# Optimization experiments

Measured on AMD Instinct MI355X. Metric: run time of the kernel, lower is better.

Reference implementation:

```python
import jax, jax.numpy as jnp
import numpy as np

NUM_HEADS = 8
NUM_LEVELS = 4
NUM_POINTS = 16
NUM_BEV = 2
EMBED = 256
BS = 64
NQ = NUM_LEVELS * NUM_POINTS  # 64


def _bilinear_sample(img, grid):
    """F.grid_sample(mode='bilinear', padding_mode='zeros', align_corners=False).
    img: (N, C, H, W); grid: (N, Hg, Wg, 2) in [-1, 1] (x, y). Returns (N, C, Hg, Wg)."""
    N, C, H, W = img.shape
    gx = (grid[..., 0] + 1.0) * (W * 0.5) - 0.5  # (N, Hg, Wg)
    gy = (grid[..., 1] + 1.0) * (H * 0.5) - 0.5
    x0 = jnp.floor(gx)
    y0 = jnp.floor(gy)
    flat = img.reshape(N, C, H * W)

    def gather(xi, yi):
        valid = (xi >= 0) & (xi <= W - 1) & (yi >= 0) & (yi <= H - 1)
        xc = jnp.clip(xi, 0, W - 1).astype(jnp.int32)
        yc = jnp.clip(yi, 0, H - 1).astype(jnp.int32)
        idx = (yc * W + xc).reshape(N, 1, -1)
        g = jnp.take_along_axis(flat, idx, axis=2).reshape(N, C, xi.shape[1], xi.shape[2])
        return g * valid[:, None, :, :].astype(img.dtype)

    wx1 = (gx - x0)[:, None]  # (N,1,Hg,Wg)
    wy1 = (gy - y0)[:, None]
    v00 = gather(x0, y0)
    v01 = gather(x0 + 1.0, y0)
    v10 = gather(x0, y0 + 1.0)
    v11 = gather(x0 + 1.0, y0 + 1.0)
    top = v00 * (1.0 - wx1) + v01 * wx1
    bot = v10 * (1.0 - wx1) + v11 * wx1
    return top * (1.0 - wy1) + bot * wy1


def _forward(query, key_hist, value_hist, reference_points, W_off, b_off, spatial_shapes):
    bs, nq, d = query.shape
    Hn, L, P, BEV = NUM_HEADS, NUM_LEVELS, NUM_POINTS, NUM_BEV
    dh = d // Hn
    Pb = P * BEV
    ss = np.asarray(spatial_shapes)  # (L, 2) static (h, w)

    queries = jnp.concatenate([query, query], axis=1)           # (bs, 2*nq, d)
    keies = jnp.concatenate([query, key_hist], axis=1)
    values = jnp.concatenate([query, value_hist], axis=1)
    qb = queries.shape[1]

    # sampling offsets projection (the only used learned linear in the original forward)
    off = (queries @ W_off + b_off).reshape(bs, qb, Hn, Pb, L, 2)

    # NOTE: original re-assigns q/k/v from the RAW concatenated tensors (to_Q/to_K/to_V discarded)
    qh = queries.reshape(bs, qb, Hn, dh)
    kh = keies.reshape(bs, qb, Hn, dh)
    vh = values.reshape(bs, qb, Hn, dh)

    attn = jax.nn.softmax(jnp.einsum('bqhd,bkhd->bqhk', qh, kh), axis=-1)
    attn = attn.reshape(bs, qb, Hn, L, Pb)

    rp = jnp.concatenate([reference_points, reference_points], axis=1)  # (bs, qb, L, 2)
    norm = jnp.stack([jnp.asarray(ss[:, 1], jnp.float32),
                      jnp.asarray(ss[:, 0], jnp.float32)], axis=-1)      # (L, 2) = (w, h)
    loc = rp[:, :, None, None, :, :] + off / norm                        # (bs,qb,H,Pb,L,2)
    # FAITHFUL: original uses .view here (pure reshape, not a transpose)
    loc = loc.reshape(bs, qb, Hn, L, Pb, 2)
    grids = 2.0 * loc - 1.0

    sampled = []
    start = 0
    for l in range(L):
        h_, w_ = int(ss[l, 0]), int(ss[l, 1])
        vl = vh[:, start:start + h_ * w_]                                # (bs, hw, H, dh)
        start += h_ * w_
        img = vl.transpose(0, 2, 3, 1).reshape(bs * Hn, dh, h_, w_)      # (bs*H, dh, h, w)
        grid_l = grids[:, :, :, l].transpose(0, 2, 1, 3, 4).reshape(bs * Hn, qb, Pb, 2)
        sampled.append(_bilinear_sample(img, grid_l))                    # (bs*H, dh, qb, Pb)

    samp = jnp.stack(sampled, axis=-2).reshape(bs * Hn, dh, qb, L * Pb)
    aw = attn.transpose(0, 2, 1, 3, 4).reshape(bs * Hn, 1, qb, L * Pb)
    out = (samp * aw).sum(-1)                                            # (bs*H, dh, qb)
    # FAITHFUL: original reshapes q_bev dim as (nq, BEV) and means over BEV
    out = out.reshape(bs, Hn * dh, nq, BEV).mean(-1).transpose(0, 2, 1)  # (bs, nq, d)
    return out + query  # dropout is identity at eval


def setup_inputs() -> dict:
    key = jax.random.key(0)
    ks = jax.random.split(key, 6)
    query = jax.random.normal(ks[0], (BS, NQ, EMBED), jnp.float32)
    key_hist = jax.random.normal(ks[1], (BS, NQ, EMBED), jnp.float32)
    value_hist = jax.random.normal(ks[2], (BS, NQ, EMBED), jnp.float32)
    reference_points = jax.random.uniform(ks[3], (BS, NQ, NUM_LEVELS, 2), jnp.float32)
    spatial_shapes = jnp.array([[4, 8]] * NUM_LEVELS, dtype=jnp.int32)  # sum(h*w)=128=L*P*BEV
    off_dim = NUM_HEADS * NUM_BEV * NUM_POINTS * NUM_LEVELS * 2
    W_off = jax.random.normal(ks[4], (EMBED, off_dim), jnp.float32) * 0.02
    b_off = jnp.zeros((off_dim,), jnp.float32)
    return {"query": query, "key_hist": key_hist, "value_hist": value_hist,
            "reference_points": reference_points, "spatial_shapes": spatial_shapes,
            "W_off": W_off, "b_off": b_off}


def reference(query, key_hist, value_hist, reference_points, spatial_shapes, W_off, b_off):
    return _forward(query, key_hist, value_hist, reference_points, W_off, b_off, spatial_shapes)
```

## Files before the change

### kernel.cpp

```cpp
#include <hip/hip_runtime.h>


typedef short  s16x8 __attribute__((ext_vector_type(8)));
typedef short  s16x4 __attribute__((ext_vector_type(4)));
typedef float  f32x4 __attribute__((ext_vector_type(4)));

__device__ __forceinline__ unsigned short f2bf(float f) {
    union { float f; unsigned u; } v; v.f = f;
    unsigned r = v.u + 0x7FFFu + ((v.u >> 16) & 1u);
    return (unsigned short)(r >> 16);
}

__global__ __launch_bounds__(256) void prep(
    const float* __restrict__ query, const float* __restrict__ key_hist,
    const float* __restrict__ value_hist,
    short* __restrict__ Ab, short* __restrict__ Khb, short* __restrict__ VTg)
{
    const int job = blockIdx.x, t = threadIdx.x;
    if (job < 2048) {
        const bool isK = job >= 1024;
        const float* src = isK ? key_hist : query;
        short* dst = isK ? Khb : Ab;
        const int i4 = ((job & 1023) * 256 + t) * 4;
        const float4 v = *(const float4*)(src + i4);
        s16x4 o;
        o.x = (short)f2bf(v.x); o.y = (short)f2bf(v.y);
        o.z = (short)f2bf(v.z); o.w = (short)f2bf(v.w);
        *(s16x4*)(dst + i4) = o;
    } else {
        const int bh = job - 2048;
        const int b = bh >> 3, h = bh & 7;
        #pragma unroll
        for (int pass = 0; pass < 4; ++pass) {
            const int idx = t + 256 * pass;
            const int p = idx >> 3;
            const int dg = idx & 7;
            const float* src = (p < 64) ? query : value_hist;
            const float4 v = *(const float4*)(src +
                (size_t)(b * 64 + (p & 63)) * 256 + h * 32 + dg * 4);
            short* o = VTg + ((size_t)bh * 32 + dg * 4) * 128 + p;
            o[0 * 128] = (short)f2bf(v.x);
            o[1 * 128] = (short)f2bf(v.y);
            o[2 * 128] = (short)f2bf(v.z);
            o[3 * 128] = (short)f2bf(v.w);
        }
    }
}

__global__ __launch_bounds__(256) void offs_gemm_mfma(
    const short* __restrict__ Ab, const float* __restrict__ W,
    const float* __restrict__ bias, short* __restrict__ OFFb)
{
    __shared__ __align__(16) short smem[128 * 136];
    short (*Asl)[40] = (short (*)[40])smem;
    short (*Bsl)[40] = (short (*)[40])(smem + 128 * 40);
    short (*Cst)[136] = (short (*)[136])smem;

    const int n0 = blockIdx.x * 128, m0 = blockIdx.y * 128;
    const int t = threadIdx.x, lane = t & 63, wave = t >> 6;
    const int wm0 = (wave >> 1) * 64, wn0 = (wave & 1) * 64;
    const int r = lane & 15, q = lane >> 4;

    f32x4 acc[4][4] = {};

    for (int kc = 0; kc < 256; kc += 32) {
        #pragma unroll
        for (int ss = 0; ss < 2; ++ss) {
            const int seg = t + ss * 256;
            const int row = seg >> 2, off8 = (seg & 3) * 8;
            *(s16x8*)&Asl[row][off8] =
                *(const s16x8*)(Ab + (size_t)(m0 + row) * 256 + kc + off8);
        }
        #pragma unroll
        for (int i = 0; i < 4; ++i) {
            const int slot = t + 256 * i;
            const int kk = slot >> 5, n4 = (slot & 31) * 4;
            const float4 w4 = *(const float4*)(W + (size_t)(kc + kk) * 2048 + n0 + n4);
            Bsl[n4 + 0][kk] = (short)f2bf(w4.x);
            Bsl[n4 + 1][kk] = (short)f2bf(w4.y);
            Bsl[n4 + 2][kk] = (short)f2bf(w4.z);
            Bsl[n4 + 3][kk] = (short)f2bf(w4.w);
        }
        __syncthreads();
        s16x8 af[4], bf[4];
        #pragma unroll
        for (int i = 0; i < 4; ++i) {
            af[i] = *(const s16x8*)&Asl[wm0 + i * 16 + r][q * 8];
            bf[i] = *(const s16x8*)&Bsl[wn0 + i * 16 + r][q * 8];
        }
        #pragma unroll
        for (int i = 0; i < 4; ++i)
            #pragma unroll
            for (int j = 0; j < 4; ++j)
                acc[i][j] = __builtin_amdgcn_mfma_f32_16x16x32_bf16(
                    af[i], bf[j], acc[i][j], 0, 0, 0);
        __syncthreads();
    }

    #pragma unroll
    for (int j = 0; j < 4; ++j) {
        const float bb = bias[n0 + wn0 + j * 16 + r];
        #pragma unroll
        for (int i = 0; i < 4; ++i)
            #pragma unroll
            for (int rg = 0; rg < 4; ++rg)
                Cst[wm0 + i * 16 + q * 4 + rg][wn0 + j * 16 + r] =
                    (short)f2bf(acc[i][j][rg] + bb);
    }
    __syncthreads();
    {
        const int row = t >> 1, half = t & 1;
        short* gdst = OFFb + (size_t)(m0 + row) * 2048 + n0 + half * 64;
        const short* lsrc = &Cst[row][half * 64];
        #pragma unroll
        for (int u = 0; u < 8; ++u)
            *(s16x8*)(gdst + u * 8) = *(const s16x8*)(lsrc + u * 8);
    }
}

__global__ __launch_bounds__(256) void fused_tsa2(
    const float* __restrict__ query, const float* __restrict__ refp,
    const short* __restrict__ Ab, const short* __restrict__ Khb,
    const short* __restrict__ VTg, const unsigned* __restrict__ OFFu,
    float* __restrict__ out)
{
    const int h = blockIdx.x, b = blockIdx.y;
    const int t = threadIdx.x, lane = t & 63, wave = t >> 6;
    const int quad = lane >> 4, col = lane & 15;
    const int wq = wave * 16;

    __shared__ __align__(16) float Am[64][132];
    short* Amb = (short*)&Am[0][0];

    unsigned off_u[8][4];
    {
        const unsigned* ob = OFFu + ((size_t)b * 64 + wq + quad * 4) * 1024 + h * 128 + col;
        #pragma unroll
        for (int r = 0; r < 4; ++r)
            #pragma unroll
            for (int t8 = 0; t8 < 8; ++t8)
                off_u[t8][r] = ob[r * 1024 + t8 * 16];
    }
    float rpx[4], rpy[4];
    #pragma unroll
    for (int r = 0; r < 4; ++r) {
        const float2 rp = *(const float2*)(refp +
            ((size_t)b * 64 + wq + quad * 4 + r) * 8 + (lane & 3) * 2);
        rpx[r] = rp.x; rpy[r] = rp.y;
    }

    {
        const int zq = t >> 2, zc = (t & 3) * 32;
        const float4 z = {0.f, 0.f, 0.f, 0.f};
        #pragma unroll
        for (int u = 0; u < 8; ++u) *(float4*)&Am[zq][zc + 4 * u] = z;
    }

    const s16x8 aq = *(const s16x8*)(Ab +
        ((size_t)b * 64 + wq + col) * 256 + h * 32 + quad * 8);
    f32x4 acc[8];
    #pragma unroll
    for (int t8 = 0; t8 < 8; ++t8) {
        const int n = t8 * 16 + col;
        const short* src = (t8 < 4)
            ? (Ab  + ((size_t)b * 64 + n) * 256)
            : (Khb + ((size_t)b * 64 + n - 64) * 256);
        const s16x8 bk = *(const s16x8*)(src + h * 32 + quad * 8);
        const f32x4 z = {0.f, 0.f, 0.f, 0.f};
        acc[t8] = __builtin_amdgcn_mfma_f32_16x16x32_bf16(aq, bk, z, 0, 0, 0);
    }

    float att[8][4];
    #pragma unroll
    for (int r = 0; r < 4; ++r) {
        float m = acc[0][r];
        #pragma unroll
        for (int t8 = 1; t8 < 8; ++t8) m = fmaxf(m, acc[t8][r]);
        #pragma unroll
        for (int s = 1; s < 16; s <<= 1) m = fmaxf(m, __shfl_xor(m, s, 64));
        float ssum = 0.f;
        #pragma unroll
        for (int t8 = 0; t8 < 8; ++t8) {
            const float e = __expf(acc[t8][r] - m);
            att[t8][r] = e; ssum += e;
        }
        #pragma unroll
        for (int s = 1; s < 16; s <<= 1) ssum += __shfl_xor(ssum, s, 64);
        const float inv = 1.0f / ssum;
        #pragma unroll
        for (int t8 = 0; t8 < 8; ++t8) att[t8][r] *= inv;
    }
    __syncthreads();

    #pragma unroll
    for (int t8 = 0; t8 < 8; ++t8) {
        const int f = col + 16 * t8;
        const int base = (f >> 5) * 32;
        #pragma unroll
        for (int r = 0; r < 4; ++r) {
            float* rowW = &Am[wq + quad * 4 + r][0];
            const float a = att[t8][r];
            const unsigned u = off_u[t8][r];
            const float ox = __uint_as_float(u << 16);
            const float oy = __uint_as_float(u & 0xFFFF0000u);
            const float gx = 8.f * (rpx[r] + ox * 0.125f) - 0.5f;
            const float gy = 4.f * (rpy[r] + oy * 0.25f) - 0.5f;
            const float x0f = floorf(gx), y0f = floorf(gy);
            const float wx = gx - x0f, wy = gy - y0f;
            const int x0 = (int)x0f, y0 = (int)y0f;
            const bool xv0 = (x0 >= 0) && (x0 < 8);
            const bool xv1 = (x0 >= -1) && (x0 < 7);
            const bool yv0 = (y0 >= 0) && (y0 < 4);
            const bool yv1 = (y0 >= -1) && (y0 < 3);
            if (xv0 && yv0) atomicAdd(&rowW[base + y0 * 8 + x0],           a * (1.f - wx) * (1.f - wy));
            if (xv1 && yv0) atomicAdd(&rowW[base + y0 * 8 + x0 + 1],       a * wx * (1.f - wy));
            if (xv0 && yv1) atomicAdd(&rowW[base + (y0 + 1) * 8 + x0],     a * (1.f - wx) * wy);
            if (xv1 && yv1) atomicAdd(&rowW[base + (y0 + 1) * 8 + x0 + 1], a * wx * wy);
        }
    }
    __syncthreads();

    {
        const int cq = t >> 2, cc = (t & 3) * 32;
        float vreg[32];
        #pragma unroll
        for (int u = 0; u < 8; ++u) {
            const float4 v = *(const float4*)&Am[cq][cc + 4 * u];
            vreg[4 * u + 0] = v.x; vreg[4 * u + 1] = v.y;
            vreg[4 * u + 2] = v.z; vreg[4 * u + 3] = v.w;
        }
        __syncthreads();
        #pragma unroll
        for (int u = 0; u < 4; ++u) {
            s16x8 o;
            #pragma unroll
            for (int j = 0; j < 8; ++j) o[j] = (short)f2bf(vreg[u * 8 + j]);
            *(s16x8*)&Amb[cq * 136 + cc + u * 8] = o;
        }
    }
    __syncthreads();

    f32x4 oacc[2] = {};
    #pragma unroll
    for (int ks = 0; ks < 4; ++ks) {
        const s16x8 af = *(const s16x8*)&Amb[(wq + col) * 136 + ks * 32 + quad * 8];
        #pragma unroll
        for (int n2 = 0; n2 < 2; ++n2) {
            const s16x8 bv = *(const s16x8*)(VTg +
                ((size_t)(b * 8 + h) * 32 + n2 * 16 + col) * 128 + ks * 32 + quad * 8);
            oacc[n2] = __builtin_amdgcn_mfma_f32_16x16x32_bf16(af, bv, oacc[n2], 0, 0, 0);
        }
    }

    #pragma unroll
    for (int n2 = 0; n2 < 2; ++n2) {
        const int d = h * 32 + n2 * 16 + col;
        #pragma unroll
        for (int pr = 0; pr < 2; ++pr) {
            const float avg = 0.5f * (oacc[n2][2 * pr] + oacc[n2][2 * pr + 1]);
            const int pj = wave * 8 + quad * 2 + pr;
            const size_t re = ((size_t)b * 64 + pj) * 256 + d;
            const size_t ro = ((size_t)b * 64 + pj + 32) * 256 + d;
            out[re] = query[re] + avg;
            out[ro] = query[ro] + avg;
        }
    }
}

extern "C" void kernel_launch(void* const* d_in, const int* in_sizes, int n_in,
                              void* d_out, int out_size, void* d_ws, size_t ws_size,
                              hipStream_t stream) {
    (void)in_sizes; (void)n_in; (void)out_size; (void)ws_size;
    const float* query      = (const float*)d_in[0];
    const float* key_hist   = (const float*)d_in[1];
    const float* value_hist = (const float*)d_in[2];
    const float* refp       = (const float*)d_in[3];
    const float* W_off      = (const float*)d_in[5];
    const float* b_off      = (const float*)d_in[6];

    char* ws = (char*)d_ws;
    short* Ab   = (short*)(ws);
    short* Khb  = (short*)(ws + (2u << 20));
    short* VTg  = (short*)(ws + (4u << 20));
    short* OFFb = (short*)(ws + (8u << 20));
    float* out  = (float*)d_out;

    prep<<<2560, 256, 0, stream>>>(query, key_hist, value_hist, Ab, Khb, VTg);
    offs_gemm_mfma<<<dim3(16, 32), 256, 0, stream>>>(Ab, W_off, b_off, OFFb);
    fused_tsa2<<<dim3(8, 64), 256, 0, stream>>>(query, refp, Ab, Khb, VTg,
                                                (const unsigned*)OFFb, out);
}
```

Measured before the change: 187.3 us.

## Fuse offset GEMM, bf16 conversion and sampling into one per-head kernel

Replaces the three-kernel pipeline (prep conversion, full offsets GEMM writing bf16 offsets to global, fused attention) with a weight transpose/convert kernel plus a single mega kernel per (head, batch). Each block converts its query/key/value slices to bf16 in LDS, computes its head's slice of the offset projection with MFMA, and consumes the offsets directly from registers for the bilinear-weight scatter. This removes the global round trip of the large offsets tensor and the intermediate bf16 buffers. The cost is heavy LDS use that limits occupancy to one block per CU, and every block of a batch redundantly converts the full query row.

```diff
diff --git a/kernel.cpp b/kernel.cpp
--- a/kernel.cpp
+++ b/kernel.cpp
@@ -11,117 +11,28 @@
     return (unsigned short)(r >> 16);
 }
 
-__global__ __launch_bounds__(256) void prep(
+__global__ __launch_bounds__(256) void transp_bf16(const float* __restrict__ W,
+                                                   short* __restrict__ Wt) {
+    __shared__ float s[32][33];
+    const int n0 = blockIdx.x * 32, k0 = blockIdx.y * 32;
+    const int c = threadIdx.x & 31, r0 = threadIdx.x >> 5;
+    #pragma unroll
+    for (int p = 0; p < 4; ++p) {
+        const int r = r0 + p * 8;
+        s[r][c] = W[(size_t)(k0 + r) * 2048 + n0 + c];
+    }
+    __syncthreads();
+    #pragma unroll
+    for (int p = 0; p < 4; ++p) {
+        const int r = r0 + p * 8;
+        Wt[(size_t)(n0 + r) * 256 + k0 + c] = (short)f2bf(s[c][r]);
+    }
+}
+
+__global__ __launch_bounds__(256, 1) void mega_tsa(
     const float* __restrict__ query, const float* __restrict__ key_hist,
-    const float* __restrict__ value_hist,
-    short* __restrict__ Ab, short* __restrict__ Khb, short* __restrict__ VTg)
-{
-    const int job = blockIdx.x, t = threadIdx.x;
-    if (job < 2048) {
-        const bool isK = job >= 1024;
-        const float* src = isK ? key_hist : query;
-        short* dst = isK ? Khb : Ab;
-        const int i4 = ((job & 1023) * 256 + t) * 4;
-        const float4 v = *(const float4*)(src + i4);
-        s16x4 o;
-        o.x = (short)f2bf(v.x); o.y = (short)f2bf(v.y);
-        o.z = (short)f2bf(v.z); o.w = (short)f2bf(v.w);
-        *(s16x4*)(dst + i4) = o;
-    } else {
-        const int bh = job - 2048;
-        const int b = bh >> 3, h = bh & 7;
-        #pragma unroll
-        for (int pass = 0; pass < 4; ++pass) {
-            const int idx = t + 256 * pass;
-            const int p = idx >> 3;
-            const int dg = idx & 7;
-            const float* src = (p < 64) ? query : value_hist;
-            const float4 v = *(const float4*)(src +
-                (size_t)(b * 64 + (p & 63)) * 256 + h * 32 + dg * 4);
-            short* o = VTg + ((size_t)bh * 32 + dg * 4) * 128 + p;
-            o[0 * 128] = (short)f2bf(v.x);
-            o[1 * 128] = (short)f2bf(v.y);
-            o[2 * 128] = (short)f2bf(v.z);
-            o[3 * 128] = (short)f2bf(v.w);
-        }
-    }
-}
-
-__global__ __launch_bounds__(256) void offs_gemm_mfma(
-    const short* __restrict__ Ab, const float* __restrict__ W,
-    const float* __restrict__ bias, short* __restrict__ OFFb)
-{
-    __shared__ __align__(16) short smem[128 * 136];
-    short (*Asl)[40] = (short (*)[40])smem;
-    short (*Bsl)[40] = (short (*)[40])(smem + 128 * 40);
-    short (*Cst)[136] = (short (*)[136])smem;
-
-    const int n0 = blockIdx.x * 128, m0 = blockIdx.y * 128;
-    const int t = threadIdx.x, lane = t & 63, wave = t >> 6;
-    const int wm0 = (wave >> 1) * 64, wn0 = (wave & 1) * 64;
-    const int r = lane & 15, q = lane >> 4;
-
-    f32x4 acc[4][4] = {};
-
-    for (int kc = 0; kc < 256; kc += 32) {
-        #pragma unroll
-        for (int ss = 0; ss < 2; ++ss) {
-            const int seg = t + ss * 256;
-            const int row = seg >> 2, off8 = (seg & 3) * 8;
-            *(s16x8*)&Asl[row][off8] =
-                *(const s16x8*)(Ab + (size_t)(m0 + row) * 256 + kc + off8);
-        }
-        #pragma unroll
-        for (int i = 0; i < 4; ++i) {
-            const int slot = t + 256 * i;
-            const int kk = slot >> 5, n4 = (slot & 31) * 4;
-            const float4 w4 = *(const float4*)(W + (size_t)(kc + kk) * 2048 + n0 + n4);
-            Bsl[n4 + 0][kk] = (short)f2bf(w4.x);
-            Bsl[n4 + 1][kk] = (short)f2bf(w4.y);
-            Bsl[n4 + 2][kk] = (short)f2bf(w4.z);
-            Bsl[n4 + 3][kk] = (short)f2bf(w4.w);
-        }
-        __syncthreads();
-        s16x8 af[4], bf[4];
-        #pragma unroll
-        for (int i = 0; i < 4; ++i) {
-            af[i] = *(const s16x8*)&Asl[wm0 + i * 16 + r][q * 8];
-            bf[i] = *(const s16x8*)&Bsl[wn0 + i * 16 + r][q * 8];
-        }
-        #pragma unroll
-        for (int i = 0; i < 4; ++i)
-            #pragma unroll
-            for (int j = 0; j < 4; ++j)
-                acc[i][j] = __builtin_amdgcn_mfma_f32_16x16x32_bf16(
-                    af[i], bf[j], acc[i][j], 0, 0, 0);
-        __syncthreads();
-    }
-
-    #pragma unroll
-    for (int j = 0; j < 4; ++j) {
-        const float bb = bias[n0 + wn0 + j * 16 + r];
-        #pragma unroll
-        for (int i = 0; i < 4; ++i)
-            #pragma unroll
-            for (int rg = 0; rg < 4; ++rg)
-                Cst[wm0 + i * 16 + q * 4 + rg][wn0 + j * 16 + r] =
-                    (short)f2bf(acc[i][j][rg] + bb);
-    }
-    __syncthreads();
-    {
-        const int row = t >> 1, half = t & 1;
-        short* gdst = OFFb + (size_t)(m0 + row) * 2048 + n0 + half * 64;
-        const short* lsrc = &Cst[row][half * 64];
-        #pragma unroll
-        for (int u = 0; u < 8; ++u)
-            *(s16x8*)(gdst + u * 8) = *(const s16x8*)(lsrc + u * 8);
-    }
-}
-
-__global__ __launch_bounds__(256) void fused_tsa2(
-    const float* __restrict__ query, const float* __restrict__ refp,
-    const short* __restrict__ Ab, const short* __restrict__ Khb,
-    const short* __restrict__ VTg, const unsigned* __restrict__ OFFu,
+    const float* __restrict__ value_hist, const float* __restrict__ refp,
+    const short* __restrict__ Wtb, const float* __restrict__ bias,
     float* __restrict__ out)
 {
     const int h = blockIdx.x, b = blockIdx.y;
@@ -129,93 +40,169 @@
     const int quad = lane >> 4, col = lane & 15;
     const int wq = wave * 16;
 
-    __shared__ __align__(16) float Am[64][132];
-    short* Amb = (short*)&Am[0][0];
-
-    unsigned off_u[8][4];
-    {
-        const unsigned* ob = OFFu + ((size_t)b * 64 + wq + quad * 4) * 1024 + h * 128 + col;
-        #pragma unroll
-        for (int r = 0; r < 4; ++r)
+    __shared__ __align__(16) short Asl[64 * 264];
+    __shared__ __align__(16) short Khl[64 * 40];
+    __shared__ __align__(16) short VTl[32 * 136];
+    __shared__ __align__(16) float attL[64 * 132];
+    __shared__ __align__(16) float rpsL[512];
+    __shared__ __align__(16) float AmU[9216];
+    short* Bsl = (short*)AmU;
+    float* Am  = AmU;
+    short* Amb = (short*)AmU;
+
+    {
+        const int row = t >> 2, seg = (t & 3) * 64;
+        const float* src = query + (size_t)(b * 64 + row) * 256 + seg;
+        #pragma unroll
+        for (int u = 0; u < 16; ++u) {
+            const float4 v = *(const float4*)(src + 4 * u);
+            s16x4 o;
+            o.x = (short)f2bf(v.x); o.y = (short)f2bf(v.y);
+            o.z = (short)f2bf(v.z); o.w = (short)f2bf(v.w);
+            *(s16x4*)&Asl[row * 264 + seg + 4 * u] = o;
+        }
+    }
+    {
+        const int row = t >> 2, s8 = (t & 3) * 8;
+        const float* src = key_hist + (size_t)(b * 64 + row) * 256 + h * 32 + s8;
+        #pragma unroll
+        for (int u = 0; u < 2; ++u) {
+            const float4 v = *(const float4*)(src + 4 * u);
+            s16x4 o;
+            o.x = (short)f2bf(v.x); o.y = (short)f2bf(v.y);
+            o.z = (short)f2bf(v.z); o.w = (short)f2bf(v.w);
+            *(s16x4*)&Khl[row * 40 + s8 + 4 * u] = o;
+        }
+    }
+    {
+        const int p = t >> 1, hf = (t & 1) * 16;
+        const float* src = ((p < 64) ? query : value_hist) +
+                           (size_t)(b * 64 + (p & 63)) * 256 + h * 32 + hf;
+        #pragma unroll
+        for (int u = 0; u < 4; ++u) {
+            const float4 v = *(const float4*)(src + 4 * u);
+            VTl[(hf + 4 * u + 0) * 136 + p] = (short)f2bf(v.x);
+            VTl[(hf + 4 * u + 1) * 136 + p] = (short)f2bf(v.y);
+            VTl[(hf + 4 * u + 2) * 136 + p] = (short)f2bf(v.z);
+            VTl[(hf + 4 * u + 3) * 136 + p] = (short)f2bf(v.w);
+        }
+    }
+    {
+        rpsL[t]       = refp[(size_t)b * 512 + t];
+        rpsL[t + 256] = refp[(size_t)b * 512 + t + 256];
+    }
+    __syncthreads();
+
+    {
+        const s16x8 aq = *(const s16x8*)&Asl[(wq + col) * 264 + h * 32 + quad * 8];
+        f32x4 lacc[8];
+        #pragma unroll
+        for (int t8 = 0; t8 < 8; ++t8) {
+            const s16x8 bk = (t8 < 4)
+                ? *(const s16x8*)&Asl[(16 * t8 + col) * 264 + h * 32 + quad * 8]
+                : *(const s16x8*)&Khl[(16 * (t8 - 4) + col) * 40 + quad * 8];
+            const f32x4 z = {0.f, 0.f, 0.f, 0.f};
+            lacc[t8] = __builtin_amdgcn_mfma_f32_16x16x32_bf16(aq, bk, z, 0, 0, 0);
+        }
+        #pragma unroll
+        for (int r = 0; r < 4; ++r) {
+            float m = lacc[0][r];
+            #pragma unroll
+            for (int t8 = 1; t8 < 8; ++t8) m = fmaxf(m, lacc[t8][r]);
+            #pragma unroll
+            for (int s = 1; s < 16; s <<= 1) m = fmaxf(m, __shfl_xor(m, s, 64));
+            float e[8], ssum = 0.f;
+            #pragma unroll
+            for (int t8 = 0; t8 < 8; ++t8) {
+                e[t8] = __expf(lacc[t8][r] - m); ssum += e[t8];
+            }
+            #pragma unroll
+            for (int s = 1; s < 16; s <<= 1) ssum += __shfl_xor(ssum, s, 64);
+            const float inv = 1.0f / ssum;
+            const int q = wq + 4 * quad + r;
             #pragma unroll
             for (int t8 = 0; t8 < 8; ++t8)
-                off_u[t8][r] = ob[r * 1024 + t8 * 16];
-    }
-    float rpx[4], rpy[4];
-    #pragma unroll
-    for (int r = 0; r < 4; ++r) {
-        const float2 rp = *(const float2*)(refp +
-            ((size_t)b * 64 + wq + quad * 4 + r) * 8 + (lane & 3) * 2);
-        rpx[r] = rp.x; rpy[r] = rp.y;
-    }
-
-    {
-        const int zq = t >> 2, zc = (t & 3) * 32;
-        const float4 z = {0.f, 0.f, 0.f, 0.f};
-        #pragma unroll
-        for (int u = 0; u < 8; ++u) *(float4*)&Am[zq][zc + 4 * u] = z;
-    }
-
-    const s16x8 aq = *(const s16x8*)(Ab +
-        ((size_t)b * 64 + wq + col) * 256 + h * 32 + quad * 8);
-    f32x4 acc[8];
-    #pragma unroll
-    for (int t8 = 0; t8 < 8; ++t8) {
-        const int n = t8 * 16 + col;
-        const short* src = (t8 < 4)
-            ? (Ab  + ((size_t)b * 64 + n) * 256)
-            : (Khb + ((size_t)b * 64 + n - 64) * 256);
-        const s16x8 bk = *(const s16x8*)(src + h * 32 + quad * 8);
-        const f32x4 z = {0.f, 0.f, 0.f, 0.f};
-        acc[t8] = __builtin_amdgcn_mfma_f32_16x16x32_bf16(aq, bk, z, 0, 0, 0);
-    }
-
-    float att[8][4];
-    #pragma unroll
-    for (int r = 0; r < 4; ++r) {
-        float m = acc[0][r];
-        #pragma unroll
-        for (int t8 = 1; t8 < 8; ++t8) m = fmaxf(m, acc[t8][r]);
-        #pragma unroll
-        for (int s = 1; s < 16; s <<= 1) m = fmaxf(m, __shfl_xor(m, s, 64));
-        float ssum = 0.f;
-        #pragma unroll
-        for (int t8 = 0; t8 < 8; ++t8) {
-            const float e = __expf(acc[t8][r] - m);
-            att[t8][r] = e; ssum += e;
-        }
-        #pragma unroll
-        for (int s = 1; s < 16; s <<= 1) ssum += __shfl_xor(ssum, s, 64);
-        const float inv = 1.0f / ssum;
-        #pragma unroll
-        for (int t8 = 0; t8 < 8; ++t8) att[t8][r] *= inv;
-    }
-    __syncthreads();
-
-    #pragma unroll
-    for (int t8 = 0; t8 < 8; ++t8) {
-        const int f = col + 16 * t8;
-        const int base = (f >> 5) * 32;
-        #pragma unroll
-        for (int r = 0; r < 4; ++r) {
-            float* rowW = &Am[wq + quad * 4 + r][0];
-            const float a = att[t8][r];
-            const unsigned u = off_u[t8][r];
-            const float ox = __uint_as_float(u << 16);
-            const float oy = __uint_as_float(u & 0xFFFF0000u);
-            const float gx = 8.f * (rpx[r] + ox * 0.125f) - 0.5f;
-            const float gy = 4.f * (rpy[r] + oy * 0.25f) - 0.5f;
-            const float x0f = floorf(gx), y0f = floorf(gy);
-            const float wx = gx - x0f, wy = gy - y0f;
-            const int x0 = (int)x0f, y0 = (int)y0f;
-            const bool xv0 = (x0 >= 0) && (x0 < 8);
-            const bool xv1 = (x0 >= -1) && (x0 < 7);
-            const bool yv0 = (y0 >= 0) && (y0 < 4);
-            const bool yv1 = (y0 >= -1) && (y0 < 3);
-            if (xv0 && yv0) atomicAdd(&rowW[base + y0 * 8 + x0],           a * (1.f - wx) * (1.f - wy));
-            if (xv1 && yv0) atomicAdd(&rowW[base + y0 * 8 + x0 + 1],       a * wx * (1.f - wy));
-            if (xv0 && yv1) atomicAdd(&rowW[base + (y0 + 1) * 8 + x0],     a * (1.f - wx) * wy);
-            if (xv1 && yv1) atomicAdd(&rowW[base + (y0 + 1) * 8 + x0 + 1], a * wx * wy);
+                attL[q * 132 + 16 * t8 + col] = e[t8] * inv;
+        }
+    }
+    __syncthreads();
+
+    f32x4 acc[4][4] = {};
+    for (int kq = 0; kq < 4; ++kq) {
+        #pragma unroll
+        for (int u = 0; u < 8; ++u) {
+            const int g = t + 256 * u;
+            const int w = g >> 9, rowu = (g >> 3) & 63, koff = (g & 7) * 8;
+            *(s16x8*)&Bsl[(w * 64 + rowu) * 72 + koff] =
+                *(const s16x8*)(Wtb + (size_t)(h * 256 + w * 64 + rowu) * 256
+                                + kq * 64 + koff);
+        }
+        __syncthreads();
+        #pragma unroll
+        for (int ks = 0; ks < 2; ++ks) {
+            const int kk = kq * 64 + ks * 32 + quad * 8;
+            s16x8 af[4], bf[4];
+            #pragma unroll
+            for (int mi = 0; mi < 4; ++mi)
+                af[mi] = *(const s16x8*)&Asl[(16 * mi + col) * 264 + kk];
+            #pragma unroll
+            for (int nj = 0; nj < 4; ++nj)
+                bf[nj] = *(const s16x8*)&Bsl[(wave * 64 + 16 * nj + col) * 72
+                                             + ks * 32 + quad * 8];
+            #pragma unroll
+            for (int mi = 0; mi < 4; ++mi)
+                #pragma unroll
+                for (int nj = 0; nj < 4; ++nj)
+                    acc[mi][nj] = __builtin_amdgcn_mfma_f32_16x16x32_bf16(
+                        af[mi], bf[nj], acc[mi][nj], 0, 0, 0);
+        }
+        __syncthreads();
+    }
+
+    {
+        #pragma unroll
+        for (int u = 0; u < 33; ++u) AmU[t + 256 * u] = 0.f;
+    }
+    __syncthreads();
+    {
+        const int i   = col >> 1;
+        const int par = col & 1;
+        const int base = 32 * wave;
+        #pragma unroll
+        for (int nj = 0; nj < 4; ++nj) {
+            const float bj = bias[h * 256 + wave * 64 + 16 * nj + col];
+            const int f = 32 * wave + 8 * nj + i;
+            #pragma unroll
+            for (int mi = 0; mi < 4; ++mi) {
+                float v[4], p[4];
+                #pragma unroll
+                for (int r = 0; r < 4; ++r) v[r] = acc[mi][nj][r] + bj;
+                #pragma unroll
+                for (int r = 0; r < 4; ++r) p[r] = __shfl_xor(v[r], 1, 64);
+                #pragma unroll
+                for (int rs = 0; rs < 2; ++rs) {
+                    const int r = par * 2 + rs;
+                    const float ox = par ? p[r] : v[r];
+                    const float oy = par ? v[r] : p[r];
+                    const int q = 16 * mi + 4 * quad + r;
+                    const float2 rp = *(const float2*)&rpsL[q * 8 + (i & 3) * 2];
+                    const float a = attL[q * 132 + f];
+                    const float gx = 8.f * (rp.x + ox * 0.125f) - 0.5f;
+                    const float gy = 4.f * (rp.y + oy * 0.25f) - 0.5f;
+                    const float x0f = floorf(gx), y0f = floorf(gy);
+                    const float wx = gx - x0f, wy = gy - y0f;
+                    const int x0 = (int)x0f, y0 = (int)y0f;
+                    float* rowW = &Am[q * 132 + base];
+                    const bool xv0 = (x0 >= 0) && (x0 < 8);
+                    const bool xv1 = (x0 >= -1) && (x0 < 7);
+                    const bool yv0 = (y0 >= 0) && (y0 < 4);
+                    const bool yv1 = (y0 >= -1) && (y0 < 3);
+                    if (xv0 && yv0) atomicAdd(&rowW[y0 * 8 + x0],           a * (1.f - wx) * (1.f - wy));
+                    if (xv1 && yv0) atomicAdd(&rowW[y0 * 8 + x0 + 1],       a * wx * (1.f - wy));
+                    if (xv0 && yv1) atomicAdd(&rowW[(y0 + 1) * 8 + x0],     a * (1.f - wx) * wy);
+                    if (xv1 && yv1) atomicAdd(&rowW[(y0 + 1) * 8 + x0 + 1], a * wx * wy);
+                }
+            }
         }
     }
     __syncthreads();
@@ -225,7 +212,7 @@
         float vreg[32];
         #pragma unroll
         for (int u = 0; u < 8; ++u) {
-            const float4 v = *(const float4*)&Am[cq][cc + 4 * u];
+            const float4 v = *(const float4*)&Am[cq * 132 + cc + 4 * u];
             vreg[4 * u + 0] = v.x; vreg[4 * u + 1] = v.y;
             vreg[4 * u + 2] = v.z; vreg[4 * u + 3] = v.w;
         }
@@ -239,30 +226,30 @@
         }
     }
     __syncthreads();
-
-    f32x4 oacc[2] = {};
-    #pragma unroll
-    for (int ks = 0; ks < 4; ++ks) {
-        const s16x8 af = *(const s16x8*)&Amb[(wq + col) * 136 + ks * 32 + quad * 8];
+    {
+        f32x4 oacc[2] = {};
+        #pragma unroll
+        for (int ks = 0; ks < 4; ++ks) {
+            const s16x8 af = *(const s16x8*)&Amb[(wq + col) * 136 + ks * 32 + quad * 8];
+            #pragma unroll
+            for (int n2 = 0; n2 < 2; ++n2) {
+                const s16x8 bv = *(const s16x8*)&VTl[(n2 * 16 + col) * 136
+                                                     + ks * 32 + quad * 8];
+                oacc[n2] = __builtin_amdgcn_mfma_f32_16x16x32_bf16(af, bv, oacc[n2], 0, 0, 0);
+            }
+        }
         #pragma unroll
         for (int n2 = 0; n2 < 2; ++n2) {
-            const s16x8 bv = *(const s16x8*)(VTg +
-                ((size_t)(b * 8 + h) * 32 + n2 * 16 + col) * 128 + ks * 32 + quad * 8);
-            oacc[n2] = __builtin_amdgcn_mfma_f32_16x16x32_bf16(af, bv, oacc[n2], 0, 0, 0);
-        }
-    }
-
-    #pragma unroll
-    for (int n2 = 0; n2 < 2; ++n2) {
-        const int d = h * 32 + n2 * 16 + col;
-        #pragma unroll
-        for (int pr = 0; pr < 2; ++pr) {
-            const float avg = 0.5f * (oacc[n2][2 * pr] + oacc[n2][2 * pr + 1]);
-            const int pj = wave * 8 + quad * 2 + pr;
-            const size_t re = ((size_t)b * 64 + pj) * 256 + d;
-            const size_t ro = ((size_t)b * 64 + pj + 32) * 256 + d;
-            out[re] = query[re] + avg;
-            out[ro] = query[ro] + avg;
+            const int d = h * 32 + n2 * 16 + col;
+            #pragma unroll
+            for (int pr = 0; pr < 2; ++pr) {
+                const float avg = 0.5f * (oacc[n2][2 * pr] + oacc[n2][2 * pr + 1]);
+                const int pj = wave * 8 + quad * 2 + pr;
+                const size_t re = ((size_t)b * 64 + pj) * 256 + d;
+                const size_t ro = ((size_t)b * 64 + pj + 32) * 256 + d;
+                out[re] = query[re] + avg;
+                out[ro] = query[ro] + avg;
+            }
         }
     }
 }
@@ -278,15 +265,10 @@
     const float* W_off      = (const float*)d_in[5];
     const float* b_off      = (const float*)d_in[6];
 
-    char* ws = (char*)d_ws;
-    short* Ab   = (short*)(ws);
-    short* Khb  = (short*)(ws + (2u << 20));
-    short* VTg  = (short*)(ws + (4u << 20));
-    short* OFFb = (short*)(ws + (8u << 20));
-    float* out  = (float*)d_out;
-
-    prep<<<2560, 256, 0, stream>>>(query, key_hist, value_hist, Ab, Khb, VTg);
-    offs_gemm_mfma<<<dim3(16, 32), 256, 0, stream>>>(Ab, W_off, b_off, OFFb);
-    fused_tsa2<<<dim3(8, 64), 256, 0, stream>>>(query, refp, Ab, Khb, VTg,
-                                                (const unsigned*)OFFb, out);
-}
+    short* Wtb = (short*)d_ws;
+    float* out = (float*)d_out;
+
+    transp_bf16<<<dim3(64, 8), 256, 0, stream>>>(W_off, Wtb);
+    mega_tsa<<<dim3(8, 64), 256, 0, stream>>>(query, key_hist, value_hist,
+                                              refp, Wtb, b_off, out);
+}
```

After: 165.4 us. 1.13x faster.

## Pre-transpose W to bf16 in prep and split scatter kernel across query halves

Applied to the files above, without the earlier changes.

The prep kernel now also transposes and converts W_off to bf16 once, so the offset GEMM loads B tiles with plain vector copies instead of strided float loads and per-element conversion. The fused attention/scatter kernel is split over two query halves, doubling the grid to raise occupancy. It stores softmax weights in LDS as bf16 and restructures the scatter so each thread handles one query row's points, using unsafeAtomicAdd for the LDS adds. The cost is redundant QK computation in waves that discard it, plus a slightly lower-precision attention weight.

```diff
diff --git a/kernel.cpp b/kernel.cpp
--- a/kernel.cpp
+++ b/kernel.cpp
@@ -10,25 +10,45 @@
     unsigned r = v.u + 0x7FFFu + ((v.u >> 16) & 1u);
     return (unsigned short)(r >> 16);
 }
+__device__ __forceinline__ float bf2f(unsigned short u) {
+    return __uint_as_float(((unsigned)u) << 16);
+}
 
 __global__ __launch_bounds__(256) void prep(
-    const float* __restrict__ query, const float* __restrict__ key_hist,
-    const float* __restrict__ value_hist,
-    short* __restrict__ Ab, short* __restrict__ Khb, short* __restrict__ VTg)
+    const float* __restrict__ W, const float* __restrict__ query,
+    const float* __restrict__ key_hist, const float* __restrict__ value_hist,
+    short* __restrict__ Wtb, short* __restrict__ Qb, short* __restrict__ Khb,
+    short* __restrict__ VTg)
 {
-    const int job = blockIdx.x, t = threadIdx.x;
-    if (job < 2048) {
-        const bool isK = job >= 1024;
+    __shared__ float s[32][33];
+    const int bx = blockIdx.x, t = threadIdx.x;
+    if (bx < 512) {
+        const int n0 = (bx & 63) * 32, k0 = (bx >> 6) * 32;
+        const int c = t & 31, r0 = t >> 5;
+        #pragma unroll
+        for (int p = 0; p < 4; ++p) {
+            const int r = r0 + p * 8;
+            s[r][c] = W[(size_t)(k0 + r) * 2048 + n0 + c];
+        }
+        __syncthreads();
+        #pragma unroll
+        for (int p = 0; p < 4; ++p) {
+            const int r = r0 + p * 8;
+            Wtb[(size_t)(n0 + r) * 256 + k0 + c] = (short)f2bf(s[c][r]);
+        }
+    } else if (bx < 2560) {
+        const int j = bx - 512;
+        const bool isK = j >= 1024;
         const float* src = isK ? key_hist : query;
-        short* dst = isK ? Khb : Ab;
-        const int i4 = ((job & 1023) * 256 + t) * 4;
+        short* dst = isK ? Khb : Qb;
+        const int i4 = ((j & 1023) * 256 + t) * 4;
         const float4 v = *(const float4*)(src + i4);
         s16x4 o;
         o.x = (short)f2bf(v.x); o.y = (short)f2bf(v.y);
         o.z = (short)f2bf(v.z); o.w = (short)f2bf(v.w);
         *(s16x4*)(dst + i4) = o;
     } else {
-        const int bh = job - 2048;
+        const int bh = bx - 2560;
         const int b = bh >> 3, h = bh & 7;
         #pragma unroll
         for (int pass = 0; pass < 4; ++pass) {
@@ -47,8 +67,8 @@
     }
 }
 
-__global__ __launch_bounds__(256) void offs_gemm_mfma(
-    const short* __restrict__ Ab, const float* __restrict__ W,
+__global__ __launch_bounds__(256) void gemm_k(
+    const short* __restrict__ Ab, const short* __restrict__ Wt,
     const float* __restrict__ bias, short* __restrict__ OFFb)
 {
     __shared__ __align__(16) short smem[128 * 136];
@@ -62,7 +82,6 @@
     const int r = lane & 15, q = lane >> 4;
 
     f32x4 acc[4][4] = {};
-
     for (int kc = 0; kc < 256; kc += 32) {
         #pragma unroll
         for (int ss = 0; ss < 2; ++ss) {
@@ -70,16 +89,8 @@
             const int row = seg >> 2, off8 = (seg & 3) * 8;
             *(s16x8*)&Asl[row][off8] =
                 *(const s16x8*)(Ab + (size_t)(m0 + row) * 256 + kc + off8);
-        }
-        #pragma unroll
-        for (int i = 0; i < 4; ++i) {
-            const int slot = t + 256 * i;
-            const int kk = slot >> 5, n4 = (slot & 31) * 4;
-            const float4 w4 = *(const float4*)(W + (size_t)(kc + kk) * 2048 + n0 + n4);
-            Bsl[n4 + 0][kk] = (short)f2bf(w4.x);
-            Bsl[n4 + 1][kk] = (short)f2bf(w4.y);
-            Bsl[n4 + 2][kk] = (short)f2bf(w4.z);
-            Bsl[n4 + 3][kk] = (short)f2bf(w4.w);
+            *(s16x8*)&Bsl[row][off8] =
+                *(const s16x8*)(Wt + (size_t)(n0 + row) * 256 + kc + off8);
         }
         __syncthreads();
         s16x8 af[4], bf[4];
@@ -96,7 +107,6 @@
                     af[i], bf[j], acc[i][j], 0, 0, 0);
         __syncthreads();
     }
-
     #pragma unroll
     for (int j = 0; j < 4; ++j) {
         const float bb = bias[n0 + wn0 + j * 16 + r];
@@ -118,120 +128,115 @@
     }
 }
 
-__global__ __launch_bounds__(256) void fused_tsa2(
+__global__ __launch_bounds__(256) void scatter_av(
     const float* __restrict__ query, const float* __restrict__ refp,
-    const short* __restrict__ Ab, const short* __restrict__ Khb,
+    const short* __restrict__ Qb, const short* __restrict__ Khb,
     const short* __restrict__ VTg, const unsigned* __restrict__ OFFu,
     float* __restrict__ out)
 {
-    const int h = blockIdx.x, b = blockIdx.y;
+    const int h = blockIdx.x, b = blockIdx.y, s = blockIdx.z;
+    const int q0 = s * 32;
     const int t = threadIdx.x, lane = t & 63, wave = t >> 6;
     const int quad = lane >> 4, col = lane & 15;
-    const int wq = wave * 16;
-
-    __shared__ __align__(16) float Am[64][132];
-    short* Amb = (short*)&Am[0][0];
-
-    unsigned off_u[8][4];
-    {
-        const unsigned* ob = OFFu + ((size_t)b * 64 + wq + quad * 4) * 1024 + h * 128 + col;
-        #pragma unroll
-        for (int r = 0; r < 4; ++r)
-            #pragma unroll
-            for (int t8 = 0; t8 < 8; ++t8)
-                off_u[t8][r] = ob[r * 1024 + t8 * 16];
-    }
-    float rpx[4], rpy[4];
-    #pragma unroll
-    for (int r = 0; r < 4; ++r) {
-        const float2 rp = *(const float2*)(refp +
-            ((size_t)b * 64 + wq + quad * 4 + r) * 8 + (lane & 3) * 2);
-        rpx[r] = rp.x; rpy[r] = rp.y;
-    }
-
-    {
-        const int zq = t >> 2, zc = (t & 3) * 32;
-        const float4 z = {0.f, 0.f, 0.f, 0.f};
-        #pragma unroll
-        for (int u = 0; u < 8; ++u) *(float4*)&Am[zq][zc + 4 * u] = z;
-    }
-
-    const s16x8 aq = *(const s16x8*)(Ab +
-        ((size_t)b * 64 + wq + col) * 256 + h * 32 + quad * 8);
-    f32x4 acc[8];
-    #pragma unroll
-    for (int t8 = 0; t8 < 8; ++t8) {
-        const int n = t8 * 16 + col;
-        const short* src = (t8 < 4)
-            ? (Ab  + ((size_t)b * 64 + n) * 256)
-            : (Khb + ((size_t)b * 64 + n - 64) * 256);
-        const s16x8 bk = *(const s16x8*)(src + h * 32 + quad * 8);
-        const f32x4 z = {0.f, 0.f, 0.f, 0.f};
-        acc[t8] = __builtin_amdgcn_mfma_f32_16x16x32_bf16(aq, bk, z, 0, 0, 0);
-    }
-
-    float att[8][4];
-    #pragma unroll
-    for (int r = 0; r < 4; ++r) {
-        float m = acc[0][r];
-        #pragma unroll
-        for (int t8 = 1; t8 < 8; ++t8) m = fmaxf(m, acc[t8][r]);
-        #pragma unroll
-        for (int s = 1; s < 16; s <<= 1) m = fmaxf(m, __shfl_xor(m, s, 64));
-        float ssum = 0.f;
+    const int mw = wave & 1;
+
+    __shared__ __align__(16) short attLb[32 * 136];
+    __shared__ __align__(16) float Am[32 * 132];
+    short* Amb = (short*)Am;
+
+    {
+        #pragma unroll
+        for (int u = 0; u < 17; ++u) {
+            const int idx = t + 256 * u;
+            if (idx < 32 * 132) Am[idx] = 0.f;
+        }
+    }
+
+    {
+        const s16x8 aq = *(const s16x8*)(Qb +
+            ((size_t)b * 64 + q0 + mw * 16 + col) * 256 + h * 32 + quad * 8);
+        f32x4 lacc[8];
         #pragma unroll
         for (int t8 = 0; t8 < 8; ++t8) {
-            const float e = __expf(acc[t8][r] - m);
-            att[t8][r] = e; ssum += e;
-        }
-        #pragma unroll
-        for (int s = 1; s < 16; s <<= 1) ssum += __shfl_xor(ssum, s, 64);
-        const float inv = 1.0f / ssum;
-        #pragma unroll
-        for (int t8 = 0; t8 < 8; ++t8) att[t8][r] *= inv;
-    }
-    __syncthreads();
-
-    #pragma unroll
-    for (int t8 = 0; t8 < 8; ++t8) {
-        const int f = col + 16 * t8;
-        const int base = (f >> 5) * 32;
-        #pragma unroll
-        for (int r = 0; r < 4; ++r) {
-            float* rowW = &Am[wq + quad * 4 + r][0];
-            const float a = att[t8][r];
-            const unsigned u = off_u[t8][r];
+            const short* src = (t8 < 4)
+                ? (Qb  + ((size_t)b * 64 + 16 * t8 + col) * 256)
+                : (Khb + ((size_t)b * 64 + 16 * (t8 - 4) + col) * 256);
+            const s16x8 bk = *(const s16x8*)(src + h * 32 + quad * 8);
+            const f32x4 z = {0.f, 0.f, 0.f, 0.f};
+            lacc[t8] = __builtin_amdgcn_mfma_f32_16x16x32_bf16(aq, bk, z, 0, 0, 0);
+        }
+        if (wave < 2) {
+            #pragma unroll
+            for (int r = 0; r < 4; ++r) {
+                float m = lacc[0][r];
+                #pragma unroll
+                for (int t8 = 1; t8 < 8; ++t8) m = fmaxf(m, lacc[t8][r]);
+                #pragma unroll
+                for (int sh = 1; sh < 16; sh <<= 1) m = fmaxf(m, __shfl_xor(m, sh, 64));
+                float e[8], ssum = 0.f;
+                #pragma unroll
+                for (int t8 = 0; t8 < 8; ++t8) {
+                    e[t8] = __expf(lacc[t8][r] - m); ssum += e[t8];
+                }
+                #pragma unroll
+                for (int sh = 1; sh < 16; sh <<= 1) ssum += __shfl_xor(ssum, sh, 64);
+                const float inv = 1.0f / ssum;
+                const int ql = mw * 16 + 4 * quad + r;
+                #pragma unroll
+                for (int t8 = 0; t8 < 8; ++t8)
+                    attLb[ql * 136 + 16 * t8 + col] = (short)f2bf(e[t8] * inv);
+            }
+        }
+    }
+    __syncthreads();
+
+    {
+        const int q = t >> 3, fg = t & 7;
+        const int qg = b * 64 + q0 + q;
+        const unsigned* offrow = OFFu + (size_t)qg * 1024 + h * 128;
+        const float* rp8 = refp + (size_t)qg * 8;
+        float rpl[8];
+        #pragma unroll
+        for (int j = 0; j < 8; ++j) rpl[j] = rp8[j];
+        float* rowW = &Am[q * 132];
+        const short* arow = &attLb[q * 136];
+        for (int i = 0; i < 16; ++i) {
+            const int f = fg + 8 * i;
+            const unsigned u = offrow[f];
             const float ox = __uint_as_float(u << 16);
             const float oy = __uint_as_float(u & 0xFFFF0000u);
-            const float gx = 8.f * (rpx[r] + ox * 0.125f) - 0.5f;
-            const float gy = 4.f * (rpy[r] + oy * 0.25f) - 0.5f;
+            const float a = bf2f((unsigned short)arow[f]);
+            const int l = f & 3;
+            const float gx = 8.f * (rpl[l * 2 + 0] + ox * 0.125f) - 0.5f;
+            const float gy = 4.f * (rpl[l * 2 + 1] + oy * 0.25f) - 0.5f;
             const float x0f = floorf(gx), y0f = floorf(gy);
             const float wx = gx - x0f, wy = gy - y0f;
             const int x0 = (int)x0f, y0 = (int)y0f;
+            const int base = (f >> 5) * 32;
             const bool xv0 = (x0 >= 0) && (x0 < 8);
             const bool xv1 = (x0 >= -1) && (x0 < 7);
             const bool yv0 = (y0 >= 0) && (y0 < 4);
             const bool yv1 = (y0 >= -1) && (y0 < 3);
-            if (xv0 && yv0) atomicAdd(&rowW[base + y0 * 8 + x0],           a * (1.f - wx) * (1.f - wy));
-            if (xv1 && yv0) atomicAdd(&rowW[base + y0 * 8 + x0 + 1],       a * wx * (1.f - wy));
-            if (xv0 && yv1) atomicAdd(&rowW[base + (y0 + 1) * 8 + x0],     a * (1.f - wx) * wy);
-            if (xv1 && yv1) atomicAdd(&rowW[base + (y0 + 1) * 8 + x0 + 1], a * wx * wy);
-        }
-    }
-    __syncthreads();
-
-    {
-        const int cq = t >> 2, cc = (t & 3) * 32;
-        float vreg[32];
-        #pragma unroll
-        for (int u = 0; u < 8; ++u) {
-            const float4 v = *(const float4*)&Am[cq][cc + 4 * u];
+            if (xv0 && yv0) unsafeAtomicAdd(&rowW[base + y0 * 8 + x0],           a * (1.f - wx) * (1.f - wy));
+            if (xv1 && yv0) unsafeAtomicAdd(&rowW[base + y0 * 8 + x0 + 1],       a * wx * (1.f - wy));
+            if (xv0 && yv1) unsafeAtomicAdd(&rowW[base + (y0 + 1) * 8 + x0],     a * (1.f - wx) * wy);
+            if (xv1 && yv1) unsafeAtomicAdd(&rowW[base + (y0 + 1) * 8 + x0 + 1], a * wx * wy);
+        }
+    }
+    __syncthreads();
+
+    {
+        const int cq = t >> 3, cc = (t & 7) * 16;
+        float vreg[16];
+        #pragma unroll
+        for (int u = 0; u < 4; ++u) {
+            const float4 v = *(const float4*)&Am[cq * 132 + cc + 4 * u];
             vreg[4 * u + 0] = v.x; vreg[4 * u + 1] = v.y;
             vreg[4 * u + 2] = v.z; vreg[4 * u + 3] = v.w;
         }
         __syncthreads();
         #pragma unroll
-        for (int u = 0; u < 4; ++u) {
+        for (int u = 0; u < 2; ++u) {
             s16x8 o;
             #pragma unroll
             for (int j = 0; j < 8; ++j) o[j] = (short)f2bf(vreg[u * 8 + j]);
@@ -240,25 +245,23 @@
     }
     __syncthreads();
 
-    f32x4 oacc[2] = {};
-    #pragma unroll
-    for (int ks = 0; ks < 4; ++ks) {
-        const s16x8 af = *(const s16x8*)&Amb[(wq + col) * 136 + ks * 32 + quad * 8];
-        #pragma unroll
-        for (int n2 = 0; n2 < 2; ++n2) {
+    {
+        const int nt = wave >> 1;
+        f32x4 oacc = {};
+        #pragma unroll
+        for (int ks = 0; ks < 4; ++ks) {
+            const s16x8 af = *(const s16x8*)&Amb[(mw * 16 + col) * 136
+                                                 + ks * 32 + quad * 8];
             const s16x8 bv = *(const s16x8*)(VTg +
-                ((size_t)(b * 8 + h) * 32 + n2 * 16 + col) * 128 + ks * 32 + quad * 8);
-            oacc[n2] = __builtin_amdgcn_mfma_f32_16x16x32_bf16(af, bv, oacc[n2], 0, 0, 0);
-        }
-    }
-
-    #pragma unroll
-    for (int n2 = 0; n2 < 2; ++n2) {
-        const int d = h * 32 + n2 * 16 + col;
+                ((size_t)(b * 8 + h) * 32 + nt * 16 + col) * 128
+                + ks * 32 + quad * 8);
+            oacc = __builtin_amdgcn_mfma_f32_16x16x32_bf16(af, bv, oacc, 0, 0, 0);
+        }
+        const int d = h * 32 + nt * 16 + col;
         #pragma unroll
         for (int pr = 0; pr < 2; ++pr) {
-            const float avg = 0.5f * (oacc[n2][2 * pr] + oacc[n2][2 * pr + 1]);
-            const int pj = wave * 8 + quad * 2 + pr;
+            const float avg = 0.5f * (oacc[2 * pr] + oacc[2 * pr + 1]);
+            const int pj = (q0 >> 1) + mw * 8 + quad * 2 + pr;
             const size_t re = ((size_t)b * 64 + pj) * 256 + d;
             const size_t ro = ((size_t)b * 64 + pj + 32) * 256 + d;
             out[re] = query[re] + avg;
@@ -279,14 +282,16 @@
     const float* b_off      = (const float*)d_in[6];
 
     char* ws = (char*)d_ws;
-    short* Ab   = (short*)(ws);
+    short* Qb   = (short*)(ws);
     short* Khb  = (short*)(ws + (2u << 20));
-    short* VTg  = (short*)(ws + (4u << 20));
-    short* OFFb = (short*)(ws + (8u << 20));
+    short* Wtb  = (short*)(ws + (4u << 20));
+    short* VTg  = (short*)(ws + (5u << 20));
+    short* OFFb = (short*)(ws + (9u << 20));
     float* out  = (float*)d_out;
 
-    prep<<<2560, 256, 0, stream>>>(query, key_hist, value_hist, Ab, Khb, VTg);
-    offs_gemm_mfma<<<dim3(16, 32), 256, 0, stream>>>(Ab, W_off, b_off, OFFb);
-    fused_tsa2<<<dim3(8, 64), 256, 0, stream>>>(query, refp, Ab, Khb, VTg,
-                                                (const unsigned*)OFFb, out);
-}
+    prep<<<3072, 256, 0, stream>>>(W_off, query, key_hist, value_hist,
+                                   Wtb, Qb, Khb, VTg);
+    gemm_k<<<dim3(16, 32), 256, 0, stream>>>(Qb, Wtb, b_off, OFFb);
+    scatter_av<<<dim3(8, 64, 2), 256, 0, stream>>>(query, refp, Qb, Khb, VTg,
+                                                   (const unsigned*)OFFb, out);
+}
```

Result: faster. 176.0 us (-6.0%).
